# Kernel tuning notes

Measured on AMD Instinct MI355X. Metric: run time of the kernel, lower is better.

## Reference

```python
import jax, jax.numpy as jnp
import numpy as np

SEQ_LEN = 720
PRED_LEN = 720
PERIOD = 24
EMB = 64
P_IN = SEQ_LEN // PERIOD            # 30
P_OUT = -(-PRED_LEN // PERIOD)      # 30 (ceil)
FREQ = EMB // 2 + 1                 # 33
DOM = (SEQ_LEN // PERIOD + 1) * 2 + 10  # 72
RATIO = PRED_LEN / SEQ_LEN          # 1.0


def _clin(z, Wr, Wi, br, bi):
    # complex nn.Linear over last dim: z @ W.T + b
    W = Wr + 1j * Wi
    b = br + 1j * bi
    return jnp.einsum('...i,oi->...o', z, W) + b


def _forward(x, freq_Wr, freq_Wi, freq_br, freq_bi, WP_W, WP_b, W_pos,
             mix1_Wr, mix1_Wi, mix1_br, mix1_bi,
             fmix_Wr, fmix_Wi, fmix_br, fmix_bi,
             proj_Wr, proj_Wi, proj_br, proj_bi,
             head_W, head_b):
    B, T, N = x.shape
    # ---- low-frequency branch ----
    low = jnp.fft.rfft(x, axis=1)[:, :DOM, :]               # [B, DOM, N] complex
    low = jnp.swapaxes(low, 1, 2)                           # [B, N, DOM]
    low = _clin(low, freq_Wr, freq_Wi, freq_br, freq_bi)    # [B, N, DOM_out]
    low = jnp.swapaxes(low, 1, 2)                           # [B, DOM_out, N]
    out_bins = PRED_LEN // 2 + 1
    low = jnp.pad(low, ((0, 0), (0, out_bins - low.shape[1]), (0, 0)))
    low_xy = jnp.fft.irfft(low, n=PRED_LEN, axis=1) * RATIO  # [B, PRED_LEN, N]

    # ---- period branch (single fixed period 24; SEQ_LEN % 24 == 0) ----
    xk = jnp.swapaxes(x, 1, 2).reshape(B, N, P_IN, PERIOD)  # unfold(size=step=24)
    xk = jnp.einsum('bnpi,oi->bnpo', xk, WP_W) + WP_b       # [B,N,P_IN,EMB]
    pf = jnp.fft.rfft(xk, axis=-1) + W_pos                  # [B,N,P_IN,FREQ] (W_pos real -> real part)
    pf = jnp.swapaxes(pf, -1, -2)                           # [B,N,FREQ,P_IN]
    o = _clin(pf, mix1_Wr, mix1_Wi, mix1_br, mix1_bi) + pf
    o = jnp.swapaxes(_clin(jnp.swapaxes(o, -1, -2), fmix_Wr, fmix_Wi, fmix_br, fmix_bi), -1, -2) + o
    o = _clin(o, proj_Wr, proj_Wi, proj_br, proj_bi)        # [B,N,FREQ,P_OUT]
    o = jnp.swapaxes(o, -1, -2)                             # [B,N,P_OUT,FREQ]
    pp = jnp.fft.irfft(o, n=EMB, axis=-1).reshape(B, N, P_OUT * EMB)
    pred = jnp.einsum('bnf,of->bno', pp, head_W) + head_b   # [B,N,PRED_LEN]
    pred = jnp.swapaxes(pred, 1, 2)                         # [B,PRED_LEN,N]
    return 0.7 * pred + 0.3 * low_xy


def setup_inputs() -> dict:
    B, N = 128, 128
    ks = jax.random.split(jax.random.key(0), 22)
    f32 = jnp.float32
    def w(k, shape, s=0.05):
        return jax.random.normal(k, shape, dtype=f32) * s
    return {
        'x': jax.random.normal(ks[0], (B, SEQ_LEN, N), dtype=f32),
        'freq_Wr': w(ks[1], (DOM, DOM)), 'freq_Wi': w(ks[2], (DOM, DOM)),
        'freq_br': w(ks[3], (DOM,)), 'freq_bi': w(ks[4], (DOM,)),
        'WP_W': w(ks[5], (EMB, PERIOD)), 'WP_b': w(ks[6], (EMB,)),
        'W_pos': jax.random.uniform(ks[7], (B, N, P_IN, FREQ), dtype=f32, minval=-0.02, maxval=0.02),
        'mix1_Wr': w(ks[8], (P_IN, P_IN)), 'mix1_Wi': w(ks[9], (P_IN, P_IN)),
        'mix1_br': w(ks[10], (P_IN,)), 'mix1_bi': w(ks[11], (P_IN,)),
        'fmix_Wr': w(ks[12], (FREQ, FREQ)), 'fmix_Wi': w(ks[13], (FREQ, FREQ)),
        'fmix_br': w(ks[14], (FREQ,)), 'fmix_bi': w(ks[15], (FREQ,)),
        'proj_Wr': w(ks[16], (P_OUT, P_IN)), 'proj_Wi': w(ks[17], (P_OUT, P_IN)),
        'proj_br': w(ks[18], (P_OUT,)), 'proj_bi': w(ks[19], (P_OUT,)),
        'head_W': w(ks[20], (PRED_LEN, P_OUT * EMB)), 'head_b': w(ks[21], (PRED_LEN,)),
    }


def reference(x, freq_Wr, freq_Wi, freq_br, freq_bi, WP_W, WP_b, W_pos,
              mix1_Wr, mix1_Wi, mix1_br, mix1_bi,
              fmix_Wr, fmix_Wi, fmix_br, fmix_bi,
              proj_Wr, proj_Wi, proj_br, proj_bi,
              head_W, head_b):
    return _forward(x, freq_Wr, freq_Wi, freq_br, freq_bi, WP_W, WP_b, W_pos,
                    mix1_Wr, mix1_Wi, mix1_br, mix1_bi,
                    fmix_Wr, fmix_Wi, fmix_br, fmix_bi,
                    proj_Wr, proj_Wi, proj_br, proj_bi,
                    head_W, head_b)
```

## Files before the change

### kernel.cpp

```cpp
#include <hip/hip_runtime.h>
#include <hip/hip_bf16.h>
#include <math.h>

#define SEQ 720
#define NCH 128
#define BATCH 128
#define BN 16384
#define DOM 72
#define PIN 30
#define POUT 30
#define FRQ 33
#define EMB 64
#define PER 24
#define KW 990
#define KP 1728
#define MT 768
#define PI_F 3.14159265358979323846f

typedef float2 cf;
__device__ __forceinline__ cf cmac(cf acc, cf a, cf b){
  acc.x += a.x*b.x - a.y*b.y; acc.y += a.x*b.y + a.y*b.x; return acc;
}
__device__ __forceinline__ short b2s(float f){
  __hip_bfloat16 h = __float2bfloat16(f);
  return *reinterpret_cast<short*>(&h);
}

__global__ __launch_bounds__(256) void p15(const float* __restrict__ WPW, const float* __restrict__ WPb,
                         const float* __restrict__ m1r, const float* __restrict__ m1i,
                         const float* __restrict__ m1br, const float* __restrict__ m1bi,
                         const float* __restrict__ fxr, const float* __restrict__ fxi,
                         const float* __restrict__ fxbr, const float* __restrict__ fxbi,
                         const float* __restrict__ pjr, const float* __restrict__ pji,
                         const float* __restrict__ pjbr, const float* __restrict__ pjbi,
                         const float* __restrict__ fqr, const float* __restrict__ fqi,
                         cf* C, cf* PM, cf* M2, cf* o3b,
                         float* __restrict__ A1r, float* __restrict__ A1i)
{
  __shared__ cf e64[64];
  __shared__ float sW[EMB*PER];
  __shared__ float sWb[EMB];
  __shared__ float sM1r[PIN*PIN], sM1i[PIN*PIN];
  __shared__ float sFxr[FRQ*FRQ], sFxi[FRQ*FRQ];
  __shared__ float sPjr[POUT*PIN], sPji[POUT*PIN];
  __shared__ float sB[6*33];
  __shared__ cf s_d[FRQ];
  __shared__ cf s_rs[PIN];
  __shared__ cf s_o1[FRQ*PIN];
  __shared__ cf s_o2[FRQ*PIN];
  __shared__ cf tbl[720];
  __shared__ cf wrow[DOM];

  int tid = threadIdx.x;
  if (blockIdx.x < DOM){
    int k = blockIdx.x;
    for (int m=tid;m<720;m+=256){ float s,c; sincosf(-2.f*PI_F*(float)m/720.f,&s,&c); tbl[m]=make_float2(c,s); }
    for (int j=tid;j<DOM;j+=256) wrow[j]=make_float2(fqr[k*DOM+j], fqi[k*DOM+j]);
    __syncthreads();
    for (int tau=tid; tau<720; tau+=256){
      cf acc=make_float2(0.f,0.f);
      for (int j=0;j<DOM;++j) acc = cmac(acc, wrow[j], tbl[(j*tau)%720]);
      A1r[k*720+tau]=acc.x;
      A1i[k*720+tau]=acc.y;
    }
    return;
  }
  if (tid < 64){ float s,c; sincosf(2.f*PI_F*tid/64.f, &s, &c); e64[tid] = make_float2(c, s); }
  for (int i=tid; i<EMB*PER; i+=256) sW[i]=WPW[i];
  if (tid < EMB) sWb[tid]=WPb[tid];
  for (int i=tid; i<PIN*PIN; i+=256){ sM1r[i]=m1r[i]; sM1i[i]=m1i[i]; sPjr[i]=pjr[i]; sPji[i]=pji[i]; }
  for (int i=tid; i<FRQ*FRQ; i+=256){ sFxr[i]=fxr[i]; sFxi[i]=fxi[i]; }
  if (tid < PIN)  { sB[tid]      = m1br[tid]; sB[33+tid]  = m1bi[tid]; }
  if (tid < FRQ)  { sB[66+tid]   = fxbr[tid]; sB[99+tid]  = fxbi[tid]; }
  if (tid < POUT) { sB[132+tid]  = pjbr[tid]; sB[165+tid] = pjbi[tid]; }
  __syncthreads();
  for (int idx=tid; idx<FRQ*PER; idx+=256){
    int f = idx/PER, i = idx%PER;
    cf acc = make_float2(0.f,0.f);
    #pragma unroll 8
    for (int o=0;o<EMB;++o){ cf e = e64[(f*o)&63]; float w = sW[o*PER+i]; acc.x += w*e.x; acc.y -= w*e.y; }
    C[idx] = acc;
  }
  for (int f=tid; f<FRQ; f+=256){
    cf acc = make_float2(0.f,0.f);
    #pragma unroll 8
    for (int o=0;o<EMB;++o){ cf e = e64[(f*o)&63]; acc.x += sWb[o]*e.x; acc.y -= sWb[o]*e.y; }
    s_d[f]=acc;
  }
  for (int idx=tid; idx<POUT*PIN; idx+=256){
    int q = idx/PIN, pp = idx%PIN;
    cf acc = make_float2(sPjr[q*PIN+pp], sPji[q*PIN+pp]);
    #pragma unroll 6
    for (int p=0;p<PIN;++p){
      cf a = make_float2(sPjr[q*PIN+p], sPji[q*PIN+p]);
      cf b = make_float2(sM1r[p*PIN+pp], sM1i[p*PIN+pp]);
      acc = cmac(acc, a, b);
    }
    PM[idx]=acc;
  }
  for (int idx=tid; idx<FRQ*FRQ; idx+=256){
    int f = idx/FRQ, ff = idx%FRQ;
    cf v = make_float2(sFxr[idx], sFxi[idx]); if (f==ff) v.x += 1.f;
    M2[idx]=v;
  }
  for (int p=tid; p<PIN; p+=256){
    cf acc = make_float2(1.f,0.f);
    #pragma unroll 6
    for (int pp=0;pp<PIN;++pp){ acc.x += sM1r[p*PIN+pp]; acc.y += sM1i[p*PIN+pp]; }
    s_rs[p]=acc;
  }
  __syncthreads();
  for (int idx=tid; idx<FRQ*PIN; idx+=256){
    int f = idx/PIN, p = idx%PIN;
    cf v = make_float2(0.f,0.f); v = cmac(v, s_d[f], s_rs[p]);
    v.x += sB[p]; v.y += sB[33+p];
    s_o1[idx]=v;
  }
  __syncthreads();
  for (int idx=tid; idx<FRQ*PIN; idx+=256){
    int f = idx/PIN, p = idx%PIN;
    cf acc = make_float2(sB[66+f], sB[99+f]);
    #pragma unroll 4
    for (int ff=0; ff<FRQ; ++ff){
      cf m2 = make_float2(sFxr[f*FRQ+ff], sFxi[f*FRQ+ff]); if (f==ff) m2.x += 1.f;
      acc = cmac(acc, m2, s_o1[ff*PIN+p]);
    }
    s_o2[idx]=acc;
  }
  __syncthreads();
  for (int idx=tid; idx<FRQ*POUT; idx+=256){
    int f = idx/POUT, q = idx%POUT;
    cf acc = make_float2(sB[132+q], sB[165+q]);
    #pragma unroll 6
    for (int p=0;p<PIN;++p){
      cf a = make_float2(sPjr[q*PIN+p], sPji[q*PIN+p]);
      acc = cmac(acc, a, s_o2[f*PIN+p]);
    }
    o3b[f*POUT+q]=acc;
  }
}

__global__ __launch_bounds__(512) void fused_mid(const float* __restrict__ hW,
                    const cf* __restrict__ PM, const cf* __restrict__ M2, const cf* __restrict__ o3b,
                    const cf* __restrict__ Cm,
                    const float* __restrict__ fbr, const float* __restrict__ fbi,
                    const float* __restrict__ headb,
                    const float* __restrict__ A1r, const float* __restrict__ A1i,
                    const float* __restrict__ x, const float* __restrict__ Wp,
                    __hip_bfloat16* __restrict__ BTm, float* __restrict__ bias,
                    __hip_bfloat16* __restrict__ Abig){
  __shared__ double smem_d[6336];
  char* smem = (char*)smem_d;
  int tid = threadIdx.x;
  int blk = blockIdx.x;

  if (blk < SEQ){
    cf*    e64 = (cf*)(smem + 0);
    float* shw = (float*)(smem + 512);
    cf*    sHc = (cf*)(smem + 8192);
    cf*    sV1 = (cf*)(smem + 16112);
    cf*    sPM = (cf*)(smem + 24032);
    cf*    sM2 = (cf*)(smem + 31232);
    cf*    sO3 = (cf*)(smem + 39944);
    float* red = (float*)(smem + 47864);
    float* sG  = (float*)(smem + 49912);
    cf* sC = (cf*)shw;
    cf* sV = sHc;
    int t = blk;
    if (tid<64){ float s,c; sincosf(2.f*PI_F*tid/64.f,&s,&c); e64[tid]=make_float2(c,s); }
    if (tid<DOM){
      int m=(tid*t)%720; float s,c; sincosf(2.f*PI_F*(float)m/720.f,&s,&c);
      float sc=(tid==0)?(1.f/720.f):(2.f/720.f);
      sG[tid]=c*sc; sG[72+tid]=s*sc;
    }
    for (int i=tid;i<1920;i+=512) shw[i]=hW[(size_t)t*1920+i];
    for (int i=tid;i<POUT*PIN;i+=512) sPM[i]=PM[i];
    for (int i=tid;i<FRQ*FRQ;i+=512) sM2[i]=M2[i];
    for (int i=tid;i<FRQ*POUT;i+=512) sO3[i]=o3b[i];
    __syncthreads();
    for (int idx=tid; idx<990; idx+=512){
      int q=idx/FRQ, f=idx%FRQ;
      cf acc=make_float2(0.f,0.f);
      const float* hw = &shw[q*64];
      #pragma unroll 8
      for (int o=0;o<EMB;++o){ cf e=e64[(f*o)&63]; float w=hw[o]; acc.x+=w*e.x; acc.y+=w*e.y; }
      float s=((f==0)||(f==32))?(1.f/64.f):(2.f/64.f);
      sHc[idx]=make_float2(acc.x*s, acc.y*s);
    }
    __syncthreads();
    for (int idx=tid; idx<990; idx+=512){
      int f=idx/PIN, p=idx%PIN;
      cf acc=make_float2(0.f,0.f);
      #pragma unroll 6
      for (int q=0;q<POUT;++q) acc=cmac(acc, sHc[q*FRQ+f], sPM[q*PIN+p]);
      sV1[idx]=acc;
    }
    float part=0.f;
    for (int idx=tid; idx<990; idx+=512){
      int q=idx/FRQ, f=idx%FRQ;
      cf h=sHc[idx]; cf o=sO3[f*POUT+q];
      part += h.x*o.x - h.y*o.y;
    }
    part *= 0.7f;
    if (tid<DOM){
      int m=(tid*t)%720; float s,c; sincosf(2.f*PI_F*(float)m/720.f,&s,&c);
      float sc=(tid==0)?(1.f/720.f):(2.f/720.f);
      part += 0.3f*sc*(c*fbr[tid] - s*fbi[tid]);
    }
    for (int i=tid;i<FRQ*PER;i+=512) sC[i]=Cm[i];
    red[tid]=part; __syncthreads();
    for (int s=256;s>0;s>>=1){ if (tid<s) red[tid]+=red[tid+s]; __syncthreads(); }
    if (tid==0) bias[t] = red[0] + 0.7f*headb[t];
    __syncthreads();
    for (int idx=tid; idx<990; idx+=512){
      int ff=idx/PIN, pp=idx%PIN;
      cf acc=make_float2(0.f,0.f);
      #pragma unroll 4
      for (int f=0;f<FRQ;++f) acc=cmac(acc, sV1[f*PIN+pp], sM2[f*FRQ+ff]);
      sV[idx]=acc;
    }
    __syncthreads();
    for (int tau=tid; tau<720; tau+=512){
      int p0 = tau/PER, i0 = tau - p0*PER;
      float mper=0.f;
      #pragma unroll 4
      for (int f=0; f<FRQ; ++f){ cf v=sV[f*PIN+p0]; cf c=sC[f*PER+i0]; mper += v.x*c.x - v.y*c.y; }
      float mlow=0.f;
      #pragma unroll 8
      for (int k=0;k<DOM;++k)
        mlow += sG[k]*A1r[k*720+tau] - sG[72+k]*A1i[k*720+tau];
      BTm[(size_t)t*KP + tau] = __float2bfloat16(0.3f*mlow + 0.7f*mper);
    }
    for (int j=tid;j<KP-SEQ;j+=512){
      float v = 0.f;
      if (j < KW){ int p=j/FRQ, f=j-p*FRQ; v = 0.7f * sV[f*PIN+p].x; }
      BTm[(size_t)t*KP + SEQ + j] = __float2bfloat16(v);
    }
    return;
  }

  if (blk < SEQ + 3072){
    float (*tile)[65] = (float(*)[65])smem;
    int bb = blk - SEQ;
    int b = bb/24; int rem = bb%24;
    int t0 = (rem>>1)*64, n0 = (rem&1)*64;
    int c = tid & 63, r0 = tid >> 6;
    #pragma unroll
    for (int s=0;s<8;++s){
      int r = r0 + s*8;
      int t = t0 + r;
      tile[r][c] = (t<SEQ) ? x[((size_t)b*SEQ + t)*NCH + n0 + c] : 0.f;
    }
    __syncthreads();
    int tq  = tid & 15;
    int nn0 = tid >> 4;
    int tt  = t0 + tq*4;
    #pragma unroll
    for (int s=0;s<2;++s){
      int nn = nn0 + s*32;
      short4 v;
      v.x = b2s(tile[tq*4+0][nn]);
      v.y = b2s(tile[tq*4+1][nn]);
      v.z = b2s(tile[tq*4+2][nn]);
      v.w = b2s(tile[tq*4+3][nn]);
      __hip_bfloat16* dst = Abig + (size_t)(b*NCH + n0+nn)*KP + tt;
      if (tt+3 < SEQ){
        *reinterpret_cast<short4*>(dst) = v;
      } else {
        short sv[4] = {v.x, v.y, v.z, v.w};
        for (int j=0;j<4;++j) if (tt+j < SEQ) *reinterpret_cast<short*>(dst+j) = sv[j];
      }
    }
    return;
  }

  {
    int bb = blk - SEQ - 3072;
    int lane8 = tid >> 6;
    int bn = bb*8 + lane8;
    int j = (tid & 63)*4;
    const float* src = Wp + (size_t)bn*KW;
    __hip_bfloat16* dstb = Abig + (size_t)bn*KP + SEQ;
    for (int jj = j; jj < KP-SEQ; jj += 256){
      float f0,f1,f2,f3;
      if (jj+3 < KW){
        float2 u = *reinterpret_cast<const float2*>(src+jj);
        float2 w = *reinterpret_cast<const float2*>(src+jj+2);
        f0=u.x; f1=u.y; f2=w.x; f3=w.y;
      } else {
        f0=(jj  <KW)?src[jj  ]:0.f; f1=(jj+1<KW)?src[jj+1]:0.f;
        f2=(jj+2<KW)?src[jj+2]:0.f; f3=(jj+3<KW)?src[jj+3]:0.f;
      }
      short4 v = { b2s(f0), b2s(f1), b2s(f2), b2s(f3) };
      *reinterpret_cast<short4*>(dstb + jj) = v;
    }
  }
}

typedef __attribute__((ext_vector_type(8))) short bfrag_t;
typedef __attribute__((ext_vector_type(4))) float accf_t;
typedef __attribute__((address_space(1))) void gvoid;
typedef __attribute__((address_space(3))) void lvoid;

__device__ __forceinline__ void gload16(const void* g, void* l){
  __builtin_amdgcn_global_load_lds((gvoid*)(g), (lvoid*)(l), 16, 0, 0);
}

__global__ __launch_bounds__(256) void gemm_main(const __hip_bfloat16* __restrict__ BTm,
                                                 const __hip_bfloat16* __restrict__ Abig,
                                                 const float* __restrict__ bias,
                                                 float* __restrict__ out)
{
  __shared__ __hip_bfloat16 At[128*32];
  __shared__ __hip_bfloat16 Bt[128*32];
  int tid = threadIdx.x;
  int lane = tid & 63;
  int wv = tid >> 6;
  int wr = wv >> 1, wc = wv & 1;
  int t0 = blockIdx.y*128, bn0 = blockIdx.x*128;

  accf_t acc[4][4];
  #pragma unroll
  for (int i=0;i<4;++i)
    #pragma unroll
    for (int j=0;j<4;++j) acc[i][j] = (accf_t){0.f,0.f,0.f,0.f};

  int lin0 = tid, lin1 = 256+tid;
  int row0 = lin0>>2, ug0 = (lin0&3) ^ ((row0>>1)&3);
  int row1 = lin1>>2, ug1 = (lin1&3) ^ ((row1>>1)&3);
  const __hip_bfloat16* gA0 = BTm  + (size_t)(t0 +row0)*KP + ug0*8;
  const __hip_bfloat16* gA1 = BTm  + (size_t)(t0 +row1)*KP + ug1*8;
  const __hip_bfloat16* gB0 = Abig + (size_t)(bn0+row0)*KP + ug0*8;
  const __hip_bfloat16* gB1 = Abig + (size_t)(bn0+row1)*KP + ug1*8;
  char* lA0 = (char*)At + lin0*16; char* lA1 = (char*)At + lin1*16;
  char* lB0 = (char*)Bt + lin0*16; char* lB1 = (char*)Bt + lin1*16;

  int g = lane>>4;
  int arow = wr*64 + (lane&15);
  int brow = wc*64 + (lane&15);

  for (int ks=0; ks<KP/32; ++ks){
    int k0 = ks*32;
    gload16(gA0 + k0, lA0);
    gload16(gA1 + k0, lA1);
    gload16(gB0 + k0, lB0);
    gload16(gB1 + k0, lB1);
    __syncthreads();
    bfrag_t af[4], bb[4];
    #pragma unroll
    for (int mi=0;mi<4;++mi){
      int r = arow + mi*16;
      int uu = g ^ ((r>>1)&3);
      af[mi] = *(const bfrag_t*)((const char*)At + r*64 + uu*16);
    }
    #pragma unroll
    for (int ni=0;ni<4;++ni){
      int r = brow + ni*16;
      int uu = g ^ ((r>>1)&3);
      bb[ni] = *(const bfrag_t*)((const char*)Bt + r*64 + uu*16);
    }
    #pragma unroll
    for (int mi=0;mi<4;++mi)
      #pragma unroll
      for (int ni=0;ni<4;++ni)
        acc[mi][ni] = __builtin_amdgcn_mfma_f32_16x16x32_bf16(af[mi], bb[ni], acc[mi][ni], 0, 0, 0);
    __syncthreads();
  }

  #pragma unroll
  for (int mi=0;mi<4;++mi){
    int tbase = t0 + wr*64 + mi*16 + (lane>>4)*4;
    #pragma unroll
    for (int ni=0;ni<4;++ni){
      int col = bn0 + wc*64 + ni*16 + (lane&15);
      int b = col>>7, n = col&127;
      size_t obase = (size_t)b*(SEQ*NCH) + n;
      #pragma unroll
      for (int r=0;r<4;++r){
        int t = tbase + r;
        if (t<SEQ) out[obase + (size_t)t*NCH] = acc[mi][ni][r] + bias[t];
      }
    }
  }
}

extern "C" void kernel_launch(void* const* d_in, const int* in_sizes, int n_in,
                              void* d_out, int out_size, void* d_ws, size_t ws_size,
                              hipStream_t stream)
{
  const float* x     = (const float*)d_in[0];
  const float* fqWr  = (const float*)d_in[1];
  const float* fqWi  = (const float*)d_in[2];
  const float* fqbr  = (const float*)d_in[3];
  const float* fqbi  = (const float*)d_in[4];
  const float* WPW   = (const float*)d_in[5];
  const float* WPb   = (const float*)d_in[6];
  const float* Wpos  = (const float*)d_in[7];
  const float* m1r   = (const float*)d_in[8];
  const float* m1i   = (const float*)d_in[9];
  const float* m1br  = (const float*)d_in[10];
  const float* m1bi  = (const float*)d_in[11];
  const float* fxr   = (const float*)d_in[12];
  const float* fxi   = (const float*)d_in[13];
  const float* fxbr  = (const float*)d_in[14];
  const float* fxbi  = (const float*)d_in[15];
  const float* pjr   = (const float*)d_in[16];
  const float* pji   = (const float*)d_in[17];
  const float* pjbr  = (const float*)d_in[18];
  const float* pjbi  = (const float*)d_in[19];
  const float* headW = (const float*)d_in[20];
  const float* headb = (const float*)d_in[21];

  char* ws = (char*)d_ws;
  size_t off = 0;
  auto alloc = [&](size_t bytes)->void*{ void* p = ws + off; off += (bytes + 255) & ~(size_t)255; return p; };
  __hip_bfloat16* Abig = (__hip_bfloat16*)alloc((size_t)BN*KP*2);
  __hip_bfloat16* BTm  = (__hip_bfloat16*)alloc((size_t)MT*KP*2);
  float* A1r = (float*)alloc((size_t)DOM*720*4);
  float* A1i = (float*)alloc((size_t)DOM*720*4);
  cf* C   = (cf*)alloc((size_t)FRQ*PER*8);
  cf* PM  = (cf*)alloc((size_t)POUT*PIN*8);
  cf* M2  = (cf*)alloc((size_t)FRQ*FRQ*8);
  cf* o3b = (cf*)alloc((size_t)FRQ*POUT*8);
  float* bias = (float*)alloc((size_t)SEQ*4);

  p15<<<DOM+1,256,0,stream>>>(WPW,WPb, m1r,m1i,m1br,m1bi, fxr,fxi,fxbr,fxbi, pjr,pji,pjbr,pjbi,
                              fqWr,fqWi, C,PM,M2,o3b, A1r,A1i);
  fused_mid<<<SEQ+3072+2048,512,0,stream>>>(headW, PM, M2, o3b, C, fqbr, fqbi, headb,
                                            A1r, A1i, x, Wpos, BTm, bias, Abig);
  gemm_main<<<dim3(128, 6), 256, 0, stream>>>(BTm, Abig, bias, (float*)d_out);
}
```

Baseline: 147.8 us.

## Double-buffer LDS tiles in bf16 MFMA GEMM to overlap loads with compute

Splits the A and B shared-memory tiles into two buffers. The main loop now issues the async global-to-LDS loads for the next K-slice before running the MFMAs on the current slice. A single barrier per iteration replaces the previous load-wait-compute-wait pattern, and a peeled epilogue handles the last slice. This aims to hide global memory latency behind matrix math, at the cost of doubled LDS use per block, which may reduce occupancy.

```diff
diff --git a/kernel.cpp b/kernel.cpp
--- a/kernel.cpp
+++ b/kernel.cpp
@@ -311,8 +311,8 @@
                                                  const float* __restrict__ bias,
                                                  float* __restrict__ out)
 {
-  __shared__ __hip_bfloat16 At[128*32];
-  __shared__ __hip_bfloat16 Bt[128*32];
+  __shared__ __hip_bfloat16 Abuf[2][128*32];
+  __shared__ __hip_bfloat16 Bbuf[2][128*32];
   int tid = threadIdx.x;
   int lane = tid & 63;
   int wv = tid >> 6;
@@ -332,32 +332,41 @@
   const __hip_bfloat16* gA1 = BTm  + (size_t)(t0 +row1)*KP + ug1*8;
   const __hip_bfloat16* gB0 = Abig + (size_t)(bn0+row0)*KP + ug0*8;
   const __hip_bfloat16* gB1 = Abig + (size_t)(bn0+row1)*KP + ug1*8;
-  char* lA0 = (char*)At + lin0*16; char* lA1 = (char*)At + lin1*16;
-  char* lB0 = (char*)Bt + lin0*16; char* lB1 = (char*)Bt + lin1*16;
+  int off0 = lin0*16, off1 = lin1*16;
 
   int g = lane>>4;
   int arow = wr*64 + (lane&15);
   int brow = wc*64 + (lane&15);
 
-  for (int ks=0; ks<KP/32; ++ks){
-    int k0 = ks*32;
-    gload16(gA0 + k0, lA0);
-    gload16(gA1 + k0, lA1);
-    gload16(gB0 + k0, lB0);
-    gload16(gB1 + k0, lB1);
-    __syncthreads();
+  gload16(gA0, (char*)Abuf[0] + off0);
+  gload16(gA1, (char*)Abuf[0] + off1);
+  gload16(gB0, (char*)Bbuf[0] + off0);
+  gload16(gB1, (char*)Bbuf[0] + off1);
+  __syncthreads();
+
+  int cur = 0;
+  for (int ks=0; ks<KP/32 - 1; ++ks){
+    int kn = (ks+1)*32;
+    char* an = (char*)Abuf[cur^1];
+    char* bn_ = (char*)Bbuf[cur^1];
+    gload16(gA0 + kn, an + off0);
+    gload16(gA1 + kn, an + off1);
+    gload16(gB0 + kn, bn_ + off0);
+    gload16(gB1 + kn, bn_ + off1);
+    const char* Ab = (const char*)Abuf[cur];
+    const char* Bb = (const char*)Bbuf[cur];
     bfrag_t af[4], bb[4];
     #pragma unroll
     for (int mi=0;mi<4;++mi){
       int r = arow + mi*16;
       int uu = g ^ ((r>>1)&3);
-      af[mi] = *(const bfrag_t*)((const char*)At + r*64 + uu*16);
+      af[mi] = *(const bfrag_t*)(Ab + r*64 + uu*16);
     }
     #pragma unroll
     for (int ni=0;ni<4;++ni){
       int r = brow + ni*16;
       int uu = g ^ ((r>>1)&3);
-      bb[ni] = *(const bfrag_t*)((const char*)Bt + r*64 + uu*16);
+      bb[ni] = *(const bfrag_t*)(Bb + r*64 + uu*16);
     }
     #pragma unroll
     for (int mi=0;mi<4;++mi)
@@ -365,6 +374,29 @@
       for (int ni=0;ni<4;++ni)
         acc[mi][ni] = __builtin_amdgcn_mfma_f32_16x16x32_bf16(af[mi], bb[ni], acc[mi][ni], 0, 0, 0);
     __syncthreads();
+    cur ^= 1;
+  }
+  {
+    const char* Ab = (const char*)Abuf[cur];
+    const char* Bb = (const char*)Bbuf[cur];
+    bfrag_t af[4], bb[4];
+    #pragma unroll
+    for (int mi=0;mi<4;++mi){
+      int r = arow + mi*16;
+      int uu = g ^ ((r>>1)&3);
+      af[mi] = *(const bfrag_t*)(Ab + r*64 + uu*16);
+    }
+    #pragma unroll
+    for (int ni=0;ni<4;++ni){
+      int r = brow + ni*16;
+      int uu = g ^ ((r>>1)&3);
+      bb[ni] = *(const bfrag_t*)(Bb + r*64 + uu*16);
+    }
+    #pragma unroll
+    for (int mi=0;mi<4;++mi)
+      #pragma unroll
+      for (int ni=0;ni<4;++ni)
+        acc[mi][ni] = __builtin_amdgcn_mfma_f32_16x16x32_bf16(af[mi], bb[ni], acc[mi][ni], 0, 0, 0);
   }
 
   #pragma unroll
```

Measured after the change: 155.6 us. 1.05x slower.

## Move input bf16 packing into precompute kernel and vectorize transpose

Applied to the files above, without the earlier changes.

The x transpose/bf16 pack and Wpos pack blocks move from the mid kernel into the first precompute kernel, so they run alongside the small weight-precompute blocks instead of after them. The per-timestep BTm construction becomes its own kernel launched after. The x transpose also switches to float4 loads and 8-wide bf16 stores with a padded tile. The aim is to overlap the large memory-bound packing work with the tiny serial precompute and to make the transpose more efficient, at the cost of a larger shared arena and a 512-thread launch for the precompute blocks.

```diff
diff --git a/kernel.cpp b/kernel.cpp
--- a/kernel.cpp
+++ b/kernel.cpp
@@ -18,6 +18,7 @@
 #define PI_F 3.14159265358979323846f
 
 typedef float2 cf;
+typedef __attribute__((ext_vector_type(8))) short short8v;
 __device__ __forceinline__ cf cmac(cf acc, cf a, cf b){
   acc.x += a.x*b.x - a.y*b.y; acc.y += a.x*b.y + a.y*b.x; return acc;
 }
@@ -26,7 +27,8 @@
   return *reinterpret_cast<short*>(&h);
 }
 
-__global__ __launch_bounds__(256) void p15(const float* __restrict__ WPW, const float* __restrict__ WPb,
+__global__ __launch_bounds__(512) void fused_pre(
+                         const float* __restrict__ WPW, const float* __restrict__ WPb,
                          const float* __restrict__ m1r, const float* __restrict__ m1i,
                          const float* __restrict__ m1br, const float* __restrict__ m1bi,
                          const float* __restrict__ fxr, const float* __restrict__ fxi,
@@ -34,30 +36,24 @@
                          const float* __restrict__ pjr, const float* __restrict__ pji,
                          const float* __restrict__ pjbr, const float* __restrict__ pjbi,
                          const float* __restrict__ fqr, const float* __restrict__ fqi,
+                         const float* __restrict__ x, const float* __restrict__ Wp,
                          cf* C, cf* PM, cf* M2, cf* o3b,
-                         float* __restrict__ A1r, float* __restrict__ A1i)
+                         float* __restrict__ A1r, float* __restrict__ A1i,
+                         __hip_bfloat16* __restrict__ Abig)
 {
-  __shared__ cf e64[64];
-  __shared__ float sW[EMB*PER];
-  __shared__ float sWb[EMB];
-  __shared__ float sM1r[PIN*PIN], sM1i[PIN*PIN];
-  __shared__ float sFxr[FRQ*FRQ], sFxi[FRQ*FRQ];
-  __shared__ float sPjr[POUT*PIN], sPji[POUT*PIN];
-  __shared__ float sB[6*33];
-  __shared__ cf s_d[FRQ];
-  __shared__ cf s_rs[PIN];
-  __shared__ cf s_o1[FRQ*PIN];
-  __shared__ cf s_o2[FRQ*PIN];
-  __shared__ cf tbl[720];
-  __shared__ cf wrow[DOM];
-
+  __shared__ double arena_d[5900];
+  char* smem = (char*)arena_d;
   int tid = threadIdx.x;
-  if (blockIdx.x < DOM){
-    int k = blockIdx.x;
-    for (int m=tid;m<720;m+=256){ float s,c; sincosf(-2.f*PI_F*(float)m/720.f,&s,&c); tbl[m]=make_float2(c,s); }
-    for (int j=tid;j<DOM;j+=256) wrow[j]=make_float2(fqr[k*DOM+j], fqi[k*DOM+j]);
-    __syncthreads();
-    for (int tau=tid; tau<720; tau+=256){
+  int blk = blockIdx.x;
+
+  if (blk < DOM){
+    cf* tbl  = (cf*)(smem);
+    cf* wrow = (cf*)(smem + 5760);
+    int k = blk;
+    for (int m=tid;m<720;m+=512){ float s,c; sincosf(-2.f*PI_F*(float)m/720.f,&s,&c); tbl[m]=make_float2(c,s); }
+    for (int j=tid;j<DOM;j+=512) wrow[j]=make_float2(fqr[k*DOM+j], fqi[k*DOM+j]);
+    __syncthreads();
+    for (int tau=tid; tau<720; tau+=512){
       cf acc=make_float2(0.f,0.f);
       for (int j=0;j<DOM;++j) acc = cmac(acc, wrow[j], tbl[(j*tau)%720]);
       A1r[k*720+tau]=acc.x;
@@ -65,217 +61,128 @@
     }
     return;
   }
-  if (tid < 64){ float s,c; sincosf(2.f*PI_F*tid/64.f, &s, &c); e64[tid] = make_float2(c, s); }
-  for (int i=tid; i<EMB*PER; i+=256) sW[i]=WPW[i];
-  if (tid < EMB) sWb[tid]=WPb[tid];
-  for (int i=tid; i<PIN*PIN; i+=256){ sM1r[i]=m1r[i]; sM1i[i]=m1i[i]; sPjr[i]=pjr[i]; sPji[i]=pji[i]; }
-  for (int i=tid; i<FRQ*FRQ; i+=256){ sFxr[i]=fxr[i]; sFxi[i]=fxi[i]; }
-  if (tid < PIN)  { sB[tid]      = m1br[tid]; sB[33+tid]  = m1bi[tid]; }
-  if (tid < FRQ)  { sB[66+tid]   = fxbr[tid]; sB[99+tid]  = fxbi[tid]; }
-  if (tid < POUT) { sB[132+tid]  = pjbr[tid]; sB[165+tid] = pjbi[tid]; }
-  __syncthreads();
-  for (int idx=tid; idx<FRQ*PER; idx+=256){
-    int f = idx/PER, i = idx%PER;
-    cf acc = make_float2(0.f,0.f);
-    #pragma unroll 8
-    for (int o=0;o<EMB;++o){ cf e = e64[(f*o)&63]; float w = sW[o*PER+i]; acc.x += w*e.x; acc.y -= w*e.y; }
-    C[idx] = acc;
-  }
-  for (int f=tid; f<FRQ; f+=256){
-    cf acc = make_float2(0.f,0.f);
-    #pragma unroll 8
-    for (int o=0;o<EMB;++o){ cf e = e64[(f*o)&63]; acc.x += sWb[o]*e.x; acc.y -= sWb[o]*e.y; }
-    s_d[f]=acc;
-  }
-  for (int idx=tid; idx<POUT*PIN; idx+=256){
-    int q = idx/PIN, pp = idx%PIN;
-    cf acc = make_float2(sPjr[q*PIN+pp], sPji[q*PIN+pp]);
-    #pragma unroll 6
-    for (int p=0;p<PIN;++p){
-      cf a = make_float2(sPjr[q*PIN+p], sPji[q*PIN+p]);
-      cf b = make_float2(sM1r[p*PIN+pp], sM1i[p*PIN+pp]);
-      acc = cmac(acc, a, b);
-    }
-    PM[idx]=acc;
-  }
-  for (int idx=tid; idx<FRQ*FRQ; idx+=256){
-    int f = idx/FRQ, ff = idx%FRQ;
-    cf v = make_float2(sFxr[idx], sFxi[idx]); if (f==ff) v.x += 1.f;
-    M2[idx]=v;
-  }
-  for (int p=tid; p<PIN; p+=256){
-    cf acc = make_float2(1.f,0.f);
-    #pragma unroll 6
-    for (int pp=0;pp<PIN;++pp){ acc.x += sM1r[p*PIN+pp]; acc.y += sM1i[p*PIN+pp]; }
-    s_rs[p]=acc;
-  }
-  __syncthreads();
-  for (int idx=tid; idx<FRQ*PIN; idx+=256){
-    int f = idx/PIN, p = idx%PIN;
-    cf v = make_float2(0.f,0.f); v = cmac(v, s_d[f], s_rs[p]);
-    v.x += sB[p]; v.y += sB[33+p];
-    s_o1[idx]=v;
-  }
-  __syncthreads();
-  for (int idx=tid; idx<FRQ*PIN; idx+=256){
-    int f = idx/PIN, p = idx%PIN;
-    cf acc = make_float2(sB[66+f], sB[99+f]);
-    #pragma unroll 4
-    for (int ff=0; ff<FRQ; ++ff){
-      cf m2 = make_float2(sFxr[f*FRQ+ff], sFxi[f*FRQ+ff]); if (f==ff) m2.x += 1.f;
-      acc = cmac(acc, m2, s_o1[ff*PIN+p]);
-    }
-    s_o2[idx]=acc;
-  }
-  __syncthreads();
-  for (int idx=tid; idx<FRQ*POUT; idx+=256){
-    int f = idx/POUT, q = idx%POUT;
-    cf acc = make_float2(sB[132+q], sB[165+q]);
-    #pragma unroll 6
-    for (int p=0;p<PIN;++p){
-      cf a = make_float2(sPjr[q*PIN+p], sPji[q*PIN+p]);
-      acc = cmac(acc, a, s_o2[f*PIN+p]);
-    }
-    o3b[f*POUT+q]=acc;
-  }
-}
-
-__global__ __launch_bounds__(512) void fused_mid(const float* __restrict__ hW,
-                    const cf* __restrict__ PM, const cf* __restrict__ M2, const cf* __restrict__ o3b,
-                    const cf* __restrict__ Cm,
-                    const float* __restrict__ fbr, const float* __restrict__ fbi,
-                    const float* __restrict__ headb,
-                    const float* __restrict__ A1r, const float* __restrict__ A1i,
-                    const float* __restrict__ x, const float* __restrict__ Wp,
-                    __hip_bfloat16* __restrict__ BTm, float* __restrict__ bias,
-                    __hip_bfloat16* __restrict__ Abig){
-  __shared__ double smem_d[6336];
-  char* smem = (char*)smem_d;
-  int tid = threadIdx.x;
-  int blk = blockIdx.x;
-
-  if (blk < SEQ){
-    cf*    e64 = (cf*)(smem + 0);
-    float* shw = (float*)(smem + 512);
-    cf*    sHc = (cf*)(smem + 8192);
-    cf*    sV1 = (cf*)(smem + 16112);
-    cf*    sPM = (cf*)(smem + 24032);
-    cf*    sM2 = (cf*)(smem + 31232);
-    cf*    sO3 = (cf*)(smem + 39944);
-    float* red = (float*)(smem + 47864);
-    float* sG  = (float*)(smem + 49912);
-    cf* sC = (cf*)shw;
-    cf* sV = sHc;
-    int t = blk;
-    if (tid<64){ float s,c; sincosf(2.f*PI_F*tid/64.f,&s,&c); e64[tid]=make_float2(c,s); }
-    if (tid<DOM){
-      int m=(tid*t)%720; float s,c; sincosf(2.f*PI_F*(float)m/720.f,&s,&c);
-      float sc=(tid==0)?(1.f/720.f):(2.f/720.f);
-      sG[tid]=c*sc; sG[72+tid]=s*sc;
-    }
-    for (int i=tid;i<1920;i+=512) shw[i]=hW[(size_t)t*1920+i];
-    for (int i=tid;i<POUT*PIN;i+=512) sPM[i]=PM[i];
-    for (int i=tid;i<FRQ*FRQ;i+=512) sM2[i]=M2[i];
-    for (int i=tid;i<FRQ*POUT;i+=512) sO3[i]=o3b[i];
-    __syncthreads();
-    for (int idx=tid; idx<990; idx+=512){
-      int q=idx/FRQ, f=idx%FRQ;
-      cf acc=make_float2(0.f,0.f);
-      const float* hw = &shw[q*64];
+
+  if (blk == DOM){
+    cf*    e64  = (cf*)(smem + 0);
+    float* sW   = (float*)(smem + 512);
+    float* sWb  = (float*)(smem + 6656);
+    float* sM1r = (float*)(smem + 6912);
+    float* sM1i = (float*)(smem + 10512);
+    float* sFxr = (float*)(smem + 14112);
+    float* sFxi = (float*)(smem + 18468);
+    float* sPjr = (float*)(smem + 22824);
+    float* sPji = (float*)(smem + 26424);
+    float* sB   = (float*)(smem + 30024);
+    cf*    s_d  = (cf*)(smem + 30816);
+    cf*    s_rs = (cf*)(smem + 31080);
+    cf*    s_o1 = (cf*)(smem + 31320);
+    cf*    s_o2 = (cf*)(smem + 39240);
+    if (tid < 64){ float s,c; sincosf(2.f*PI_F*tid/64.f, &s, &c); e64[tid] = make_float2(c, s); }
+    for (int i=tid; i<EMB*PER; i+=512) sW[i]=WPW[i];
+    if (tid < EMB) sWb[tid]=WPb[tid];
+    for (int i=tid; i<PIN*PIN; i+=512){ sM1r[i]=m1r[i]; sM1i[i]=m1i[i]; sPjr[i]=pjr[i]; sPji[i]=pji[i]; }
+    for (int i=tid; i<FRQ*FRQ; i+=512){ sFxr[i]=fxr[i]; sFxi[i]=fxi[i]; }
+    if (tid < PIN)  { sB[tid]      = m1br[tid]; sB[33+tid]  = m1bi[tid]; }
+    if (tid < FRQ)  { sB[66+tid]   = fxbr[tid]; sB[99+tid]  = fxbi[tid]; }
+    if (tid < POUT) { sB[132+tid]  = pjbr[tid]; sB[165+tid] = pjbi[tid]; }
+    __syncthreads();
+    for (int idx=tid; idx<FRQ*PER; idx+=512){
+      int f = idx/PER, i = idx%PER;
+      cf acc = make_float2(0.f,0.f);
       #pragma unroll 8
-      for (int o=0;o<EMB;++o){ cf e=e64[(f*o)&63]; float w=hw[o]; acc.x+=w*e.x; acc.y+=w*e.y; }
-      float s=((f==0)||(f==32))?(1.f/64.f):(2.f/64.f);
-      sHc[idx]=make_float2(acc.x*s, acc.y*s);
-    }
-    __syncthreads();
-    for (int idx=tid; idx<990; idx+=512){
-      int f=idx/PIN, p=idx%PIN;
-      cf acc=make_float2(0.f,0.f);
+      for (int o=0;o<EMB;++o){ cf e = e64[(f*o)&63]; float w = sW[o*PER+i]; acc.x += w*e.x; acc.y -= w*e.y; }
+      C[idx] = acc;
+    }
+    for (int f=tid; f<FRQ; f+=512){
+      cf acc = make_float2(0.f,0.f);
+      #pragma unroll 8
+      for (int o=0;o<EMB;++o){ cf e = e64[(f*o)&63]; acc.x += sWb[o]*e.x; acc.y -= sWb[o]*e.y; }
+      s_d[f]=acc;
+    }
+    for (int idx=tid; idx<POUT*PIN; idx+=512){
+      int q = idx/PIN, pp = idx%PIN;
+      cf acc = make_float2(sPjr[q*PIN+pp], sPji[q*PIN+pp]);
       #pragma unroll 6
-      for (int q=0;q<POUT;++q) acc=cmac(acc, sHc[q*FRQ+f], sPM[q*PIN+p]);
-      sV1[idx]=acc;
-    }
-    float part=0.f;
-    for (int idx=tid; idx<990; idx+=512){
-      int q=idx/FRQ, f=idx%FRQ;
-      cf h=sHc[idx]; cf o=sO3[f*POUT+q];
-      part += h.x*o.x - h.y*o.y;
-    }
-    part *= 0.7f;
-    if (tid<DOM){
-      int m=(tid*t)%720; float s,c; sincosf(2.f*PI_F*(float)m/720.f,&s,&c);
-      float sc=(tid==0)?(1.f/720.f):(2.f/720.f);
-      part += 0.3f*sc*(c*fbr[tid] - s*fbi[tid]);
-    }
-    for (int i=tid;i<FRQ*PER;i+=512) sC[i]=Cm[i];
-    red[tid]=part; __syncthreads();
-    for (int s=256;s>0;s>>=1){ if (tid<s) red[tid]+=red[tid+s]; __syncthreads(); }
-    if (tid==0) bias[t] = red[0] + 0.7f*headb[t];
-    __syncthreads();
-    for (int idx=tid; idx<990; idx+=512){
-      int ff=idx/PIN, pp=idx%PIN;
-      cf acc=make_float2(0.f,0.f);
+      for (int p=0;p<PIN;++p){
+        cf a = make_float2(sPjr[q*PIN+p], sPji[q*PIN+p]);
+        cf b = make_float2(sM1r[p*PIN+pp], sM1i[p*PIN+pp]);
+        acc = cmac(acc, a, b);
+      }
+      PM[idx]=acc;
+    }
+    for (int idx=tid; idx<FRQ*FRQ; idx+=512){
+      int f = idx/FRQ, ff = idx%FRQ;
+      cf v = make_float2(sFxr[idx], sFxi[idx]); if (f==ff) v.x += 1.f;
+      M2[idx]=v;
+    }
+    for (int p=tid; p<PIN; p+=512){
+      cf acc = make_float2(1.f,0.f);
+      #pragma unroll 6
+      for (int pp=0;pp<PIN;++pp){ acc.x += sM1r[p*PIN+pp]; acc.y += sM1i[p*PIN+pp]; }
+      s_rs[p]=acc;
+    }
+    __syncthreads();
+    for (int idx=tid; idx<FRQ*PIN; idx+=512){
+      int f = idx/PIN, p = idx%PIN;
+      cf v = make_float2(0.f,0.f); v = cmac(v, s_d[f], s_rs[p]);
+      v.x += sB[p]; v.y += sB[33+p];
+      s_o1[idx]=v;
+    }
+    __syncthreads();
+    for (int idx=tid; idx<FRQ*PIN; idx+=512){
+      int f = idx/PIN, p = idx%PIN;
+      cf acc = make_float2(sB[66+f], sB[99+f]);
       #pragma unroll 4
-      for (int f=0;f<FRQ;++f) acc=cmac(acc, sV1[f*PIN+pp], sM2[f*FRQ+ff]);
-      sV[idx]=acc;
-    }
-    __syncthreads();
-    for (int tau=tid; tau<720; tau+=512){
-      int p0 = tau/PER, i0 = tau - p0*PER;
-      float mper=0.f;
-      #pragma unroll 4
-      for (int f=0; f<FRQ; ++f){ cf v=sV[f*PIN+p0]; cf c=sC[f*PER+i0]; mper += v.x*c.x - v.y*c.y; }
-      float mlow=0.f;
-      #pragma unroll 8
-      for (int k=0;k<DOM;++k)
-        mlow += sG[k]*A1r[k*720+tau] - sG[72+k]*A1i[k*720+tau];
-      BTm[(size_t)t*KP + tau] = __float2bfloat16(0.3f*mlow + 0.7f*mper);
-    }
-    for (int j=tid;j<KP-SEQ;j+=512){
-      float v = 0.f;
-      if (j < KW){ int p=j/FRQ, f=j-p*FRQ; v = 0.7f * sV[f*PIN+p].x; }
-      BTm[(size_t)t*KP + SEQ + j] = __float2bfloat16(v);
+      for (int ff=0; ff<FRQ; ++ff){
+        cf m2 = make_float2(sFxr[f*FRQ+ff], sFxi[f*FRQ+ff]); if (f==ff) m2.x += 1.f;
+        acc = cmac(acc, m2, s_o1[ff*PIN+p]);
+      }
+      s_o2[idx]=acc;
+    }
+    __syncthreads();
+    for (int idx=tid; idx<FRQ*POUT; idx+=512){
+      int f = idx/POUT, q = idx%POUT;
+      cf acc = make_float2(sB[132+q], sB[165+q]);
+      #pragma unroll 6
+      for (int p=0;p<PIN;++p){
+        cf a = make_float2(sPjr[q*PIN+p], sPji[q*PIN+p]);
+        acc = cmac(acc, a, s_o2[f*PIN+p]);
+      }
+      o3b[f*POUT+q]=acc;
     }
     return;
   }
 
-  if (blk < SEQ + 3072){
-    float (*tile)[65] = (float(*)[65])smem;
-    int bb = blk - SEQ;
+  if (blk < DOM + 1 + 3072){
+    float (*tile)[68] = (float(*)[68])smem;
+    int bb = blk - (DOM+1);
     int b = bb/24; int rem = bb%24;
     int t0 = (rem>>1)*64, n0 = (rem&1)*64;
-    int c = tid & 63, r0 = tid >> 6;
-    #pragma unroll
-    for (int s=0;s<8;++s){
-      int r = r0 + s*8;
+    int r0 = tid >> 4;
+    int c4 = (tid & 15)*4;
+    #pragma unroll
+    for (int s=0;s<2;++s){
+      int r = r0 + s*32;
       int t = t0 + r;
-      tile[r][c] = (t<SEQ) ? x[((size_t)b*SEQ + t)*NCH + n0 + c] : 0.f;
-    }
-    __syncthreads();
-    int tq  = tid & 15;
-    int nn0 = tid >> 4;
-    int tt  = t0 + tq*4;
-    #pragma unroll
-    for (int s=0;s<2;++s){
-      int nn = nn0 + s*32;
-      short4 v;
-      v.x = b2s(tile[tq*4+0][nn]);
-      v.y = b2s(tile[tq*4+1][nn]);
-      v.z = b2s(tile[tq*4+2][nn]);
-      v.w = b2s(tile[tq*4+3][nn]);
-      __hip_bfloat16* dst = Abig + (size_t)(b*NCH + n0+nn)*KP + tt;
-      if (tt+3 < SEQ){
-        *reinterpret_cast<short4*>(dst) = v;
-      } else {
-        short sv[4] = {v.x, v.y, v.z, v.w};
-        for (int j=0;j<4;++j) if (tt+j < SEQ) *reinterpret_cast<short*>(dst+j) = sv[j];
-      }
+      float4 v = make_float4(0.f,0.f,0.f,0.f);
+      if (t < SEQ) v = *reinterpret_cast<const float4*>(&x[((size_t)b*SEQ + t)*NCH + n0 + c4]);
+      *reinterpret_cast<float4*>(&tile[r][c4]) = v;
+    }
+    __syncthreads();
+    int n  = tid & 63;
+    int tg = tid >> 6;
+    int tt = tg*8;
+    if (t0 + tt < SEQ){
+      short8v v;
+      #pragma unroll
+      for (int j=0;j<8;++j) v[j] = b2s(tile[tt+j][n]);
+      *reinterpret_cast<short8v*>(Abig + (size_t)(b*NCH + n0+n)*KP + t0 + tt) = v;
     }
     return;
   }
 
   {
-    int bb = blk - SEQ - 3072;
+    int bb = blk - (DOM+1) - 3072;
     int lane8 = tid >> 6;
     int bn = bb*8 + lane8;
     int j = (tid & 63)*4;
@@ -294,6 +201,99 @@
       short4 v = { b2s(f0), b2s(f1), b2s(f2), b2s(f3) };
       *reinterpret_cast<short4*>(dstb + jj) = v;
     }
+  }
+}
+
+__global__ __launch_bounds__(512) void p_big3(const float* __restrict__ hW,
+                    const cf* __restrict__ PM, const cf* __restrict__ M2, const cf* __restrict__ o3b,
+                    const cf* __restrict__ Cm,
+                    const float* __restrict__ fbr, const float* __restrict__ fbi,
+                    const float* __restrict__ headb,
+                    const float* __restrict__ A1r, const float* __restrict__ A1i,
+                    __hip_bfloat16* __restrict__ BTm, float* __restrict__ bias){
+  __shared__ double smem_d[6336];
+  char* smem = (char*)smem_d;
+  int tid = threadIdx.x;
+  cf*    e64 = (cf*)(smem + 0);
+  float* shw = (float*)(smem + 512);
+  cf*    sHc = (cf*)(smem + 8192);
+  cf*    sV1 = (cf*)(smem + 16112);
+  cf*    sPM = (cf*)(smem + 24032);
+  cf*    sM2 = (cf*)(smem + 31232);
+  cf*    sO3 = (cf*)(smem + 39944);
+  float* red = (float*)(smem + 47864);
+  float* sG  = (float*)(smem + 49912);
+  cf* sC = (cf*)shw;
+  cf* sV = sHc;
+  int t = blockIdx.x;
+  if (tid<64){ float s,c; sincosf(2.f*PI_F*tid/64.f,&s,&c); e64[tid]=make_float2(c,s); }
+  if (tid<DOM){
+    int m=(tid*t)%720; float s,c; sincosf(2.f*PI_F*(float)m/720.f,&s,&c);
+    float sc=(tid==0)?(1.f/720.f):(2.f/720.f);
+    sG[tid]=c*sc; sG[72+tid]=s*sc;
+  }
+  for (int i=tid;i<1920;i+=512) shw[i]=hW[(size_t)t*1920+i];
+  for (int i=tid;i<POUT*PIN;i+=512) sPM[i]=PM[i];
+  for (int i=tid;i<FRQ*FRQ;i+=512) sM2[i]=M2[i];
+  for (int i=tid;i<FRQ*POUT;i+=512) sO3[i]=o3b[i];
+  __syncthreads();
+  for (int idx=tid; idx<990; idx+=512){
+    int q=idx/FRQ, f=idx%FRQ;
+    cf acc=make_float2(0.f,0.f);
+    const float* hw = &shw[q*64];
+    #pragma unroll 8
+    for (int o=0;o<EMB;++o){ cf e=e64[(f*o)&63]; float w=hw[o]; acc.x+=w*e.x; acc.y+=w*e.y; }
+    float s=((f==0)||(f==32))?(1.f/64.f):(2.f/64.f);
+    sHc[idx]=make_float2(acc.x*s, acc.y*s);
+  }
+  __syncthreads();
+  for (int idx=tid; idx<990; idx+=512){
+    int f=idx/PIN, p=idx%PIN;
+    cf acc=make_float2(0.f,0.f);
+    #pragma unroll 6
+    for (int q=0;q<POUT;++q) acc=cmac(acc, sHc[q*FRQ+f], sPM[q*PIN+p]);
+    sV1[idx]=acc;
+  }
+  float part=0.f;
+  for (int idx=tid; idx<990; idx+=512){
+    int q=idx/FRQ, f=idx%FRQ;
+    cf h=sHc[idx]; cf o=sO3[f*POUT+q];
+    part += h.x*o.x - h.y*o.y;
+  }
+  part *= 0.7f;
+  if (tid<DOM){
+    int m=(tid*t)%720; float s,c; sincosf(2.f*PI_F*(float)m/720.f,&s,&c);
+    float sc=(tid==0)?(1.f/720.f):(2.f/720.f);
+    part += 0.3f*sc*(c*fbr[tid] - s*fbi[tid]);
+  }
+  for (int i=tid;i<FRQ*PER;i+=512) sC[i]=Cm[i];
+  red[tid]=part; __syncthreads();
+  for (int s=256;s>0;s>>=1){ if (tid<s) red[tid]+=red[tid+s]; __syncthreads(); }
+  if (tid==0) bias[t] = red[0] + 0.7f*headb[t];
+  __syncthreads();
+  for (int idx=tid; idx<990; idx+=512){
+    int ff=idx/PIN, pp=idx%PIN;
+    cf acc=make_float2(0.f,0.f);
+    #pragma unroll 4
+    for (int f=0;f<FRQ;++f) acc=cmac(acc, sV1[f*PIN+pp], sM2[f*FRQ+ff]);
+    sV[idx]=acc;
+  }
+  __syncthreads();
+  for (int tau=tid; tau<720; tau+=512){
+    int p0 = tau/PER, i0 = tau - p0*PER;
+    float mper=0.f;
+    #pragma unroll 4
+    for (int f=0; f<FRQ; ++f){ cf v=sV[f*PIN+p0]; cf c=sC[f*PER+i0]; mper += v.x*c.x - v.y*c.y; }
+    float mlow=0.f;
+    #pragma unroll 8
+    for (int k=0;k<DOM;++k)
+      mlow += sG[k]*A1r[k*720+tau] - sG[72+k]*A1i[k*720+tau];
+    BTm[(size_t)t*KP + tau] = __float2bfloat16(0.3f*mlow + 0.7f*mper);
+  }
+  for (int j=tid;j<KP-SEQ;j+=512){
+    float v = 0.f;
+    if (j < KW){ int p=j/FRQ, f=j-p*FRQ; v = 0.7f * sV[f*PIN+p].x; }
+    BTm[(size_t)t*KP + SEQ + j] = __float2bfloat16(v);
   }
 }
 
@@ -424,9 +424,9 @@
   cf* o3b = (cf*)alloc((size_t)FRQ*POUT*8);
   float* bias = (float*)alloc((size_t)SEQ*4);
 
-  p15<<<DOM+1,256,0,stream>>>(WPW,WPb, m1r,m1i,m1br,m1bi, fxr,fxi,fxbr,fxbi, pjr,pji,pjbr,pjbi,
-                              fqWr,fqWi, C,PM,M2,o3b, A1r,A1i);
-  fused_mid<<<SEQ+3072+2048,512,0,stream>>>(headW, PM, M2, o3b, C, fqbr, fqbi, headb,
-                                            A1r, A1i, x, Wpos, BTm, bias, Abig);
+  fused_pre<<<DOM+1+3072+2048,512,0,stream>>>(WPW,WPb, m1r,m1i,m1br,m1bi, fxr,fxi,fxbr,fxbi,
+                                              pjr,pji,pjbr,pjbi, fqWr,fqWi, x, Wpos,
+                                              C,PM,M2,o3b, A1r,A1i, Abig);
+  p_big3<<<SEQ,512,0,stream>>>(headW, PM, M2, o3b, C, fqbr, fqbi, headb, A1r, A1i, BTm, bias);
   gemm_main<<<dim3(128, 6), 256, 0, stream>>>(BTm, Abig, bias, (float*)d_out);
 }
```

Measured after the change: 128.6 us. 13.0% less time.
